# Kernel tuning notes

Hardware: AMD Instinct MI355X
Metric: run time of the kernel (lower is better)

## Reference

```python
import jax, jax.numpy as jnp
import numpy as np
from math import comb

B = 2048          # num_batch
NVAR = 11         # Bernstein coefficients per axis
NUM = 100         # trajectory time samples
NUM_OBS = 10
MAXITER = 50
T_FIN = 5.0
A_OBS = 0.4; B_OBS = 0.4
RHO_OBS = 1.0; RHO_INEQ = 1.0; RHO_TARGET = 1.0; RHO_PROJ = 1.0
V_MIN = 0.1; V_MAX = 2.0; A_MAX = 2.0


def _bernstein(n, t):
    return np.stack([comb(n, k) * t**k * (1.0 - t)**(n - k) for k in range(n + 1)], axis=1)


def _basis_matrices():
    # Bernstein polynomial basis of degree NVAR-1 sampled at NUM points over [0, T_FIN]
    t = np.linspace(0.0, 1.0, NUM)
    n = NVAR - 1
    P = _bernstein(n, t)
    Bm1 = _bernstein(n - 1, t)
    Bm2 = _bernstein(n - 2, t)
    dP = np.zeros_like(P); ddP = np.zeros_like(P)
    for k in range(n + 1):
        d = np.zeros(NUM)
        if k > 0: d += Bm1[:, k - 1]
        if k < n: d -= Bm1[:, k]
        dP[:, k] = n * d / T_FIN
        dd = np.zeros(NUM)
        if k > 1: dd += Bm2[:, k - 2]
        if 0 < k < n: dd -= 2.0 * Bm2[:, k - 1]
        if k < n - 1: dd += Bm2[:, k]
        ddP[:, k] = n * (n - 1) * dd / T_FIN**2
    return (jnp.asarray(P, jnp.float32), jnp.asarray(dP, jnp.float32), jnp.asarray(ddP, jnp.float32))


def setup_inputs() -> dict:
    key = jax.random.key(0)
    ks = jax.random.split(key, 10)
    P, Pdot, Pddot = _basis_matrices()
    u = lambda k, s, lo, hi: jax.random.uniform(k, s, jnp.float32, lo, hi)
    init_state_ego = jnp.concatenate([u(ks[0], (B, 2), -1.0, 1.0), u(ks[1], (B, 2), 0.1, 1.0)], axis=1)
    term_states = jnp.concatenate([u(ks[2], (B, 2), 2.0, 6.0), u(ks[3], (B, 2), 0.1, 1.0)], axis=1)
    via_points = u(ks[4], (B, 4), 0.5, 4.0)
    closest_obs = u(ks[5], (B, 2 * NUM_OBS), -4.0, 4.0)
    target_init = jnp.concatenate([u(ks[6], (B, 2), 1.0, 5.0), u(ks[7], (B, 2), -0.5, 0.5)], axis=1)
    d_min_t = u(ks[8], (B, 1), 1.0, 1.5)
    d_max_t = d_min_t + u(ks[9], (B, 1), 0.5, 1.0)
    d_target_bounds = jnp.concatenate([d_min_t, d_max_t], axis=1)
    return {"P": P, "Pdot": Pdot, "Pddot": Pddot, "init_state_ego": init_state_ego,
            "term_states": term_states, "via_points": via_points, "closest_obs": closest_obs,
            "target_init": target_init, "d_target_bounds": d_target_bounds}


def reference(P, Pdot, Pddot, init_state_ego, term_states, via_points, closest_obs, target_init, d_target_bounds):
    dt = P.dtype
    tot_time = jnp.linspace(0.0, T_FIN, NUM, dtype=dt)
    A_via = jnp.stack([P[49], P[74]])
    A_eq_init = jnp.vstack([P[0], Pdot[0], P[-1], Pdot[-1], A_via])   # [6, NVAR]
    A_eq = jnp.vstack([P[0], Pdot[0], P[-1], Pdot[-1]])               # [4, NVAR]
    A_obs_mat = jnp.tile(P, (NUM_OBS, 1))                             # [NUM_OBS*NUM, NVAR]
    A_vel, A_acc, A_target = Pdot, Pddot, P

    def kkt_inv(cost, A):
        m = A.shape[0]
        M = jnp.vstack([jnp.hstack([cost, A.T]), jnp.hstack([A, jnp.zeros((m, m), dt)])])
        return jnp.linalg.inv(M)

    inv_init = kkt_inv(Pddot.T @ Pddot, A_eq_init)
    cost_opt = (RHO_OBS * A_obs_mat.T @ A_obs_mat + RHO_INEQ * A_acc.T @ A_acc
                + RHO_INEQ * A_vel.T @ A_vel + RHO_TARGET * A_target.T @ A_target
                + RHO_PROJ * jnp.eye(NVAR, dtype=dt))
    inv_opt = kkt_inv(cost_opt, A_eq)

    zeros1 = jnp.zeros((B, 1), dt)
    vx0, vy0 = init_state_ego[:, 2:3], init_state_ego[:, 3:4]
    x_term, y_term = term_states[:, 0:1], term_states[:, 1:2]
    vx_term, vy_term = term_states[:, 2:3], term_states[:, 3:4]

    # warm-start QP (equality-constrained, zero linear cost): qp_layer_init
    b_eq_x_init = jnp.hstack([zeros1, vx0, x_term, vx_term, via_points[:, 0:2]])
    b_eq_y_init = jnp.hstack([zeros1, vy0, y_term, vy_term, via_points[:, 2:4]])
    zlin = jnp.zeros((B, NVAR), dt)
    c_x_bar = (jnp.hstack([zlin, b_eq_x_init]) @ inv_init.T)[:, :NVAR]
    c_y_bar = (jnp.hstack([zlin, b_eq_y_init]) @ inv_init.T)[:, :NVAR]

    b_eq_x = jnp.hstack([zeros1, vx0, x_term, vx_term])
    b_eq_y = jnp.hstack([zeros1, vy0, y_term, vy_term])

    # constant-velocity target trajectory, [B, NUM]
    x_target = target_init[:, 0:1] + target_init[:, 2:3] * tot_time[None, :]
    y_target = target_init[:, 1:2] + target_init[:, 3:4] * tot_time[None, :]

    # static obstacles tiled over time (obs-major, time fastest), [B, NUM_OBS*NUM]
    x_obs_traj = jnp.repeat(closest_obs[:, :NUM_OBS], NUM, axis=1)
    y_obs_traj = jnp.repeat(closest_obs[:, NUM_OBS:2 * NUM_OBS], NUM, axis=1)
    d_min_t, d_max_t = d_target_bounds[:, 0:1], d_target_bounds[:, 1:2]

    def step(carry, _):
        primal, lx, ly = carry
        cx, cy = primal[:, :NVAR], primal[:, NVAR:]
        x, xdot, xddot = cx @ P.T, cx @ Pdot.T, cx @ Pddot.T
        y, ydot, yddot = cy @ P.T, cy @ Pdot.T, cy @ Pddot.T
        # obstacle avoidance polar reformulation (compute_alph_d)
        wc = jnp.tile(x, (1, NUM_OBS)) - x_obs_traj
        ws = jnp.tile(y, (1, NUM_OBS)) - y_obs_traj
        a_o = jnp.arctan2(ws * A_OBS, wc * B_OBS)
        ca, sa = jnp.cos(a_o), jnp.sin(a_o)
        c1 = RHO_OBS * (A_OBS**2 * ca**2 + B_OBS**2 * sa**2)
        c2 = RHO_OBS * (A_OBS * wc * ca + B_OBS * ws * sa)
        d_obs = jnp.maximum(jnp.ones_like(c2), c2 / c1)
        # velocity bound (rho_ineq cancels in c2/c1)
        a_v = jnp.arctan2(ydot, xdot); cv, sv = jnp.cos(a_v), jnp.sin(a_v)
        d_v = jnp.clip(xdot * cv + ydot * sv, V_MIN, V_MAX)
        # acceleration bound
        a_a = jnp.arctan2(yddot, xddot); cA, sA = jnp.cos(a_a), jnp.sin(a_a)
        d_a = jnp.clip(xddot * cA + yddot * sA, 0.0, A_MAX)
        # target distance band
        wct, wst = x - x_target, y - y_target
        bt = jnp.arctan2(wst, wct); cb, sb = jnp.cos(bt), jnp.sin(bt)
        d_t = jnp.clip(wct * cb + wst * sb, d_min_t, d_max_t)
        # residuals -> dual (lambda) update
        res_xo = wc - A_OBS * d_obs * ca; res_yo = ws - B_OBS * d_obs * sa
        res_vx = xdot - d_v * cv;         res_vy = ydot - d_v * sv
        res_ax = xddot - d_a * cA;        res_ay = yddot - d_a * sA
        res_tx = wct - d_t * cb;          res_ty = wst - d_t * sb
        lx = lx - RHO_OBS * res_xo @ A_obs_mat - RHO_INEQ * res_ax @ A_acc - RHO_INEQ * res_vx @ A_vel - RHO_TARGET * res_tx @ A_target
        ly = ly - RHO_OBS * res_yo @ A_obs_mat - RHO_INEQ * res_ay @ A_acc - RHO_INEQ * res_vy @ A_vel - RHO_TARGET * res_ty @ A_target
        # linear cost and closed-form KKT solve (A_projection = I)
        b_ox = x_obs_traj + A_OBS * d_obs * ca; b_oy = y_obs_traj + B_OBS * d_obs * sa
        b_tx = x_target + d_t * cb;             b_ty = y_target + d_t * sb
        lin_x = (-lx - RHO_OBS * b_ox @ A_obs_mat - RHO_INEQ * (d_a * cA) @ A_acc
                 - RHO_INEQ * (d_v * cv) @ A_vel - RHO_TARGET * b_tx @ A_target - RHO_PROJ * c_x_bar)
        lin_y = (-ly - RHO_OBS * b_oy @ A_obs_mat - RHO_INEQ * (d_a * sA) @ A_acc
                 - RHO_INEQ * (d_v * sv) @ A_vel - RHO_TARGET * b_ty @ A_target - RHO_PROJ * c_y_bar)
        new_cx = (jnp.hstack([-lin_x, b_eq_x]) @ inv_opt.T)[:, :NVAR]
        new_cy = (jnp.hstack([-lin_y, b_eq_y]) @ inv_opt.T)[:, :NVAR]
        return (jnp.hstack([new_cx, new_cy]), lx, ly), None

    init = (jnp.hstack([c_x_bar, c_y_bar]), jnp.zeros((B, NVAR), dt), jnp.zeros((B, NVAR), dt))
    (primal, lx, ly), _ = jax.lax.scan(jax.checkpoint(step), init, None, length=MAXITER)
    return primal
```

## Files before the change

kernel.cpp:

```cpp
#include <hip/hip_runtime.h>
#include <math.h>

#define NVARS 11
#define NUMT  100
#define NOBS  10
#define MAXIT 50

#define E_OFF    0
#define F_OFF    66
#define G4_OFF   187
#define GP_OFF   231
#define GPD_OFF  352
#define GPDD_OFF 473
#define WS_FLOATS 594

#define BSTRIDE 308

__device__ void gj_inv(double (*aug)[34], int N, double* fac, int* piv, int tid, int nthr)
{
    for (int k = 0; k < N; ++k) {
        if (tid == 0) {
            int p = k; double best = fabs(aug[k][k]);
            for (int r = k + 1; r < N; ++r) { double v = fabs(aug[r][k]); if (v > best) { best = v; p = r; } }
            *piv = p;
        }
        __syncthreads();
        int p = *piv;
        if (p != k) {
            for (int c = tid; c < 2 * N; c += nthr) { double t = aug[k][c]; aug[k][c] = aug[p][c]; aug[p][c] = t; }
        }
        __syncthreads();
        double pv = aug[k][k];
        __syncthreads();
        for (int c = tid; c < 2 * N; c += nthr) aug[k][c] /= pv;
        __syncthreads();
        if (tid < N) fac[tid] = aug[tid][k];
        __syncthreads();
        for (int idx = tid; idx < N * 2 * N; idx += nthr) {
            int r = idx / (2 * N), c = idx % (2 * N);
            if (r != k) aug[r][c] -= fac[r] * aug[k][c];
        }
        __syncthreads();
    }
}

__global__ __launch_bounds__(128) void setup_kernel(const float* __restrict__ P,
                                                    const float* __restrict__ Pd,
                                                    const float* __restrict__ Pdd,
                                                    float* __restrict__ ws)
{
    __shared__ double G[3][NVARS][NVARS];
    __shared__ double aug[17][34];
    __shared__ double fac[17];
    __shared__ int piv;
    const int tid = threadIdx.x, nthr = 128;

    for (int idx = tid; idx < 3 * 121; idx += nthr) {
        int q = idx / 121, rem = idx % 121, r = rem / 11, c = rem % 11;
        const float* B = (q == 0) ? P : (q == 1) ? Pd : Pdd;
        double s = 0.0;
        for (int t = 0; t < NUMT; ++t) s += (double)B[t * 11 + r] * (double)B[t * 11 + c];
        G[q][r][c] = s;
    }
    __syncthreads();
    for (int idx = tid; idx < 3 * 121; idx += nthr) ws[GP_OFF + idx] = (float)((&G[0][0][0])[idx]);

    for (int idx = tid; idx < 17 * 34; idx += nthr) aug[idx / 34][idx % 34] = 0.0;
    __syncthreads();
    for (int idx = tid; idx < 121; idx += nthr) aug[idx / 11][idx % 11] = G[2][idx / 11][idx % 11];
    if (tid < 66) {
        int r = tid / 11, j = tid % 11;
        const float* src = (r == 0) ? P : (r == 1) ? Pd : (r == 2) ? (P + 99 * 11) : (r == 3) ? (Pd + 99 * 11)
                           : (r == 4) ? (P + 49 * 11) : (P + 74 * 11);
        double v = (double)src[j];
        aug[j][11 + r] = v;
        aug[11 + r][j] = v;
    }
    if (tid < 17) aug[tid][17 + tid] = 1.0;
    __syncthreads();
    gj_inv(aug, 17, fac, &piv, tid, nthr);
    if (tid < 66) { int j = tid / 6, k = tid % 6; ws[E_OFF + tid] = (float)aug[j][17 + 11 + k]; }
    __syncthreads();

    for (int idx = tid; idx < 17 * 34; idx += nthr) aug[idx / 34][idx % 34] = 0.0;
    __syncthreads();
    for (int idx = tid; idx < 121; idx += nthr) {
        int r = idx / 11, c = idx % 11;
        aug[r][c] = 11.0 * G[0][r][c] + G[1][r][c] + G[2][r][c] + ((r == c) ? 1.0 : 0.0);
    }
    if (tid < 44) {
        int r = tid / 11, j = tid % 11;
        const float* src = (r == 0) ? P : (r == 1) ? Pd : (r == 2) ? (P + 99 * 11) : (Pd + 99 * 11);
        double v = (double)src[j];
        aug[j][11 + r] = v;
        aug[11 + r][j] = v;
    }
    if (tid < 15) aug[tid][15 + tid] = 1.0;
    __syncthreads();
    gj_inv(aug, 15, fac, &piv, tid, nthr);
    if (tid < 121) { int j = tid / 11, k = tid % 11; ws[F_OFF + tid] = (float)aug[j][15 + k]; }
    if (tid < 44)  { int j = tid / 4,  k = tid % 4;  ws[G4_OFF + tid] = (float)aug[j][15 + 11 + k]; }
}

__device__ __forceinline__ float sbcast(float v) {
    return __int_as_float(__builtin_amdgcn_readfirstlane(__float_as_int(v)));
}

__global__ __launch_bounds__(128, 4) void solve_kernel(
    const float* __restrict__ P, const float* __restrict__ Pd, const float* __restrict__ Pdd,
    const float* __restrict__ ise, const float* __restrict__ term, const float* __restrict__ via,
    const float* __restrict__ obs, const float* __restrict__ tgt, const float* __restrict__ dtb,
    const float* __restrict__ ws, float* __restrict__ out)
{
    __shared__ __align__(16) float sBc[NVARS][BSTRIDE];
    __shared__ __align__(16) float wbc[2][BSTRIDE];
    __shared__ float cst[WS_FLOATS];
    __shared__ float sd456[3][24];
    __shared__ float Dred[6][12];
    __shared__ float mlin[2][12];
    __shared__ float scoef[2][12];
    __shared__ float beqs[2][4];
    __shared__ float sobs[2][NOBS];
    __shared__ float stgt[6];

    const int tid = threadIdx.x;
    const int b = blockIdx.x;

    for (int idx = tid; idx < NVARS * BSTRIDE; idx += 128) {
        int j = idx / BSTRIDE, r = idx % BSTRIDE;
        float v = 0.f;
        if (r < 300) {
            int q = r / 100, t = r % 100;
            const float* Bq = (q == 0) ? P : (q == 1) ? Pd : Pdd;
            v = Bq[t * 11 + j];
        }
        sBc[j][r] = v;
    }
    for (int idx = tid; idx < WS_FLOATS; idx += 128) cst[idx] = ws[idx];
    if (tid < 20) sobs[tid / 10][tid % 10] = obs[b * 20 + tid];
    if (tid == 0) {
        beqs[0][0] = 0.f; beqs[0][1] = ise[b*4+2]; beqs[0][2] = term[b*4+0]; beqs[0][3] = term[b*4+2];
        beqs[1][0] = 0.f; beqs[1][1] = ise[b*4+3]; beqs[1][2] = term[b*4+1]; beqs[1][3] = term[b*4+3];
        stgt[0] = tgt[b*4+0]; stgt[1] = tgt[b*4+2];
        stgt[2] = tgt[b*4+1]; stgt[3] = tgt[b*4+3];
        stgt[4] = dtb[b*2+0]; stgt[5] = dtb[b*2+1];
    }
    __syncthreads();

    const int ca = tid / 11, cj = tid % 11;
    float lm = 0.f, cb = 0.f;
    if (tid < 22) {
        float bi0 = 0.f, bi1 = beqs[ca][1], bi2 = beqs[ca][2], bi3 = beqs[ca][3];
        float bi4 = via[b*4 + 2*ca + 0], bi5 = via[b*4 + 2*ca + 1];
        const float* E = &cst[E_OFF + cj * 6];
        float s = E[0]*bi0 + E[1]*bi1 + E[2]*bi2 + E[3]*bi3 + E[4]*bi4 + E[5]*bi5;
        cb = s; scoef[ca][cj] = s;
    }

    float rP[NVARS], rPd[NVARS], rPdd[NVARS];
    {
        const int t = (tid < NUMT) ? tid : 0;
        #pragma unroll
        for (int k = 0; k < NVARS; ++k) {
            rP[k]   = sBc[k][t];
            rPd[k]  = sBc[k][t + 100];
            rPdd[k] = sBc[k][t + 200];
        }
    }
    float obx[NOBS], oby[NOBS];
    #pragma unroll
    for (int o = 0; o < NOBS; ++o) {
        obx[o] = sbcast(sobs[0][o]);
        oby[o] = sbcast(sobs[1][o]);
    }
    const float tg0 = sbcast(stgt[0]), tg1 = sbcast(stgt[1]);
    const float tg2 = sbcast(stgt[2]), tg3 = sbcast(stgt[3]);
    const float tg4 = sbcast(stgt[4]), tg5 = sbcast(stgt[5]);

    float* pwA = &wbc[0][tid];
    const int lg = tid - 100;

    int btask = -1;
    if (tid <= 32) btask = tid;
    else if (tid >= 64 && tid <= 96) btask = tid - 31;
    const int wi = (btask >= 0) ? btask % 6 : 0;
    const int bjj = (btask >= 0) ? btask / 6 : 0;
    const float4* pbB = (const float4*)(&sBc[0][0] + bjj * BSTRIDE + (wi % 3) * 100);
    const float4* pwB = (const float4*)(&wbc[wi / 3][(wi % 3) * 100]);
    __syncthreads();

    for (int it = 0; it < MAXIT; ++it) {
        if (tid < NUMT) {
            float x=0,y=0,xd=0,yd=0,xdd=0,ydd=0;
            #pragma unroll
            for (int k = 0; k < NVARS; ++k) {
                float cxk = scoef[0][k], cyk = scoef[1][k];
                x += cxk*rP[k];   y += cyk*rP[k];
                xd += cxk*rPd[k]; yd += cyk*rPd[k];
                xdd += cxk*rPdd[k]; ydd += cyk*rPdd[k];
            }
            float Sbx = 0.f, Sby = 0.f;
            #pragma unroll
            for (int o = 0; o < NOBS; ++o) {
                float dx = x - obx[o], dy = y - oby[o];
                float r2 = dx*dx + dy*dy;
                float f  = fmaxf(1.0f, 0.4f * rsqrtf(fmaxf(r2, 1e-30f)));
                Sbx += fmaf(dx, f, obx[o]);
                Sby += fmaf(dy, f, oby[o]);
            }
            float rv = sqrtf(xd*xd + yd*yd);
            float fv = fminf(fmaxf(rv, 0.1f), 2.0f) / fmaxf(rv, 1e-30f);
            float ra = sqrtf(xdd*xdd + ydd*ydd);
            float fa = fminf(ra, 2.0f) / fmaxf(ra, 1e-30f);
            float tt = (float)tid * (5.0f / 99.0f);
            float xt = tg0 + tg1*tt, yt = tg2 + tg3*tt;
            float wct = x - xt, wst = y - yt;
            float rt = sqrtf(wct*wct + wst*wst);
            float ftg = fminf(fmaxf(rt, tg4), tg5) / fmaxf(rt, 1e-30f);
            pwA[0]   = Sbx + xt + wct*ftg;
            pwA[100] = xd * fv;
            pwA[200] = xdd * fa;
            pwA[BSTRIDE]       = Sby + yt + wst*ftg;
            pwA[BSTRIDE + 100] = yd * fv;
            pwA[BSTRIDE + 200] = ydd * fa;
        }
        if (lg >= 0 && lg < 22) {
            const int ga = lg / 11, gj = lg % 11;
            float d4=0.f, d5=0.f, d6=0.f;
            #pragma unroll
            for (int k = 0; k < 11; ++k) {
                float ck = scoef[ga][k];
                d4 += ck * cst[GP_OFF   + k*11 + gj];
                d5 += ck * cst[GPD_OFF  + k*11 + gj];
                d6 += ck * cst[GPDD_OFF + k*11 + gj];
            }
            sd456[0][lg] = d4; sd456[1][lg] = d5; sd456[2][lg] = d6;
        }
        __syncthreads();

        if (btask >= 0) {
            float s = 0.f;
            #pragma unroll
            for (int i = 0; i < 25; ++i) {
                float4 a = pbB[i], w = pwB[i];
                s += w.x * a.x; s += w.y * a.y; s += w.z * a.z; s += w.w * a.w;
            }
            Dred[wi][bjj] = s;
        }
        __syncthreads();

        if (tid < 22) {
            float d4 = sd456[0][tid], d5 = sd456[1][tid], d6 = sd456[2][tid];
            int i0 = 3*ca;
            float D0 = Dred[i0][cj], D1 = Dred[i0+1][cj], D2 = Dred[i0+2][cj];
            lm -= (11.f*d4 - D0) + (d5 - D1) + (d6 - D2);
            mlin[ca][cj] = lm + D0 + D1 + D2 + cb;
        }

        if (tid < 22) {
            float s = 0.f;
            #pragma unroll
            for (int k = 0; k < 11; ++k) s += cst[F_OFF + cj*11 + k] * mlin[ca][k];
            #pragma unroll
            for (int k = 0; k < 4; ++k)  s += cst[G4_OFF + cj*4 + k] * beqs[ca][k];
            scoef[ca][cj] = s;
        }
        __syncthreads();
    }

    if (tid < 22) out[b * 22 + tid] = scoef[ca][cj];
}

extern "C" void kernel_launch(void* const* d_in, const int* in_sizes, int n_in,
                              void* d_out, int out_size, void* d_ws, size_t ws_size,
                              hipStream_t stream)
{
    const float* P    = (const float*)d_in[0];
    const float* Pd   = (const float*)d_in[1];
    const float* Pdd  = (const float*)d_in[2];
    const float* ise  = (const float*)d_in[3];
    const float* term = (const float*)d_in[4];
    const float* via  = (const float*)d_in[5];
    const float* obs  = (const float*)d_in[6];
    const float* tgt  = (const float*)d_in[7];
    const float* dtb  = (const float*)d_in[8];
    float* ws  = (float*)d_ws;
    float* out = (float*)d_out;

    const int B = in_sizes[3] / 4;

    hipLaunchKernelGGL(setup_kernel, dim3(1), dim3(128), 0, stream, P, Pd, Pdd, ws);
    hipLaunchKernelGGL(solve_kernel, dim3(B), dim3(128), 0, stream,
                       P, Pd, Pdd, ise, term, via, obs, tgt, dtb, ws, out);
}
```

Before: 240.7 us.

## Split Bernstein reduction dot products across all threads in two halves

The 66 length-100 reduction dot products were computed by 66 threads, each doing 25 float4 iterations. Now every one of the 128 threads computes half of a dot product (12-13 float4s), with four threads taking an extra half, and the partial sums go to shared memory and are added in the coefficient update. The d4/d5/d6 and coefficient-update work also moves from threads 0-21 to threads 100-121, so those values stay in registers and one shared buffer goes away. This shortens the critical path of the reduction stage at the cost of a few extra shared-memory reads and some index arithmetic.

Measured after the change: 246.8 us. 1.03x slower.

```diff
diff --git a/kernel.cpp b/kernel.cpp
--- a/kernel.cpp
+++ b/kernel.cpp
@@ -115,8 +115,7 @@
     __shared__ __align__(16) float sBc[NVARS][BSTRIDE];
     __shared__ __align__(16) float wbc[2][BSTRIDE];
     __shared__ float cst[WS_FLOATS];
-    __shared__ float sd456[3][24];
-    __shared__ float Dred[6][12];
+    __shared__ float pS[136];
     __shared__ float mlin[2][12];
     __shared__ float scoef[2][12];
     __shared__ float beqs[2][4];
@@ -147,9 +146,11 @@
     }
     __syncthreads();
 
-    const int ca = tid / 11, cj = tid % 11;
+    const int lc = tid - 100;
+    const int ca = (lc >= 0) ? lc / 11 : 0, cj = (lc >= 0) ? lc % 11 : 0;
+
     float lm = 0.f, cb = 0.f;
-    if (tid < 22) {
+    if (lc >= 0 && lc < 22) {
         float bi0 = 0.f, bi1 = beqs[ca][1], bi2 = beqs[ca][2], bi3 = beqs[ca][3];
         float bi4 = via[b*4 + 2*ca + 0], bi5 = via[b*4 + 2*ca + 1];
         const float* E = &cst[E_OFF + cj * 6];
@@ -178,16 +179,22 @@
     const float tg4 = sbcast(stgt[4]), tg5 = sbcast(stgt[5]);
 
     float* pwA = &wbc[0][tid];
-    const int lg = tid - 100;
-
-    int btask = -1;
-    if (tid <= 32) btask = tid;
-    else if (tid >= 64 && tid <= 96) btask = tid - 31;
-    const int wi = (btask >= 0) ? btask % 6 : 0;
-    const int bjj = (btask >= 0) ? btask / 6 : 0;
-    const float4* pbB = (const float4*)(&sBc[0][0] + bjj * BSTRIDE + (wi % 3) * 100);
-    const float4* pwB = (const float4*)(&wbc[wi / 3][(wi % 3) * 100]);
-    __syncthreads();
+
+    const int sB   = tid;
+    const int taskB = (sB < 66) ? sB : sB - 66;
+    const int halfB = (sB < 66) ? 0 : 1;
+    const int wiB = taskB % 6, bjB = taskB / 6;
+    const float4* pbB = (const float4*)(&sBc[0][0] + bjB * BSTRIDE + (wiB % 3) * 100) + (halfB ? 13 : 0);
+    const float4* pwB = (const float4*)(&wbc[wiB / 3][(wiB % 3) * 100]) + (halfB ? 13 : 0);
+    const int ccB = halfB ? 12 : 13;
+    const bool has2 = (tid >= 60 && tid < 64);
+    const int task2 = 62 + (tid - 60);
+    const int wi2 = task2 % 6, bj2 = task2 / 6;
+    const float4* pb2 = (const float4*)(&sBc[0][0] + bj2 * BSTRIDE + (wi2 % 3) * 100) + 13;
+    const float4* pw2 = (const float4*)(&wbc[wi2 / 3][(wi2 % 3) * 100]) + 13;
+    __syncthreads();
+
+    float d4 = 0.f, d5 = 0.f, d6 = 0.f;
 
     for (int it = 0; it < MAXIT; ++it) {
         if (tid < NUMT) {
@@ -224,40 +231,54 @@
             pwA[BSTRIDE + 100] = yd * fv;
             pwA[BSTRIDE + 200] = ydd * fa;
         }
-        if (lg >= 0 && lg < 22) {
-            const int ga = lg / 11, gj = lg % 11;
-            float d4=0.f, d5=0.f, d6=0.f;
+        if (lc >= 0 && lc < 22) {
+            float a4=0.f, a5=0.f, a6=0.f;
             #pragma unroll
             for (int k = 0; k < 11; ++k) {
-                float ck = scoef[ga][k];
-                d4 += ck * cst[GP_OFF   + k*11 + gj];
-                d5 += ck * cst[GPD_OFF  + k*11 + gj];
-                d6 += ck * cst[GPDD_OFF + k*11 + gj];
-            }
-            sd456[0][lg] = d4; sd456[1][lg] = d5; sd456[2][lg] = d6;
-        }
-        __syncthreads();
-
-        if (btask >= 0) {
+                float ck = scoef[ca][k];
+                a4 += ck * cst[GP_OFF   + k*11 + cj];
+                a5 += ck * cst[GPD_OFF  + k*11 + cj];
+                a6 += ck * cst[GPDD_OFF + k*11 + cj];
+            }
+            d4 = a4; d5 = a5; d6 = a6;
+        }
+        __syncthreads();
+
+        {
             float s = 0.f;
             #pragma unroll
-            for (int i = 0; i < 25; ++i) {
-                float4 a = pbB[i], w = pwB[i];
+            for (int i = 0; i < 13; ++i) {
+                if (i < ccB) {
+                    float4 a = pbB[i], w = pwB[i];
+                    s += w.x * a.x; s += w.y * a.y; s += w.z * a.z; s += w.w * a.w;
+                }
+            }
+            pS[sB] = s;
+        }
+        if (has2) {
+            float s = 0.f;
+            #pragma unroll
+            for (int i = 0; i < 12; ++i) {
+                float4 a = pb2[i], w = pw2[i];
                 s += w.x * a.x; s += w.y * a.y; s += w.z * a.z; s += w.w * a.w;
             }
-            Dred[wi][bjj] = s;
-        }
-        __syncthreads();
-
-        if (tid < 22) {
-            float d4 = sd456[0][tid], d5 = sd456[1][tid], d6 = sd456[2][tid];
-            int i0 = 3*ca;
-            float D0 = Dred[i0][cj], D1 = Dred[i0+1][cj], D2 = Dred[i0+2][cj];
+            pS[128 + (tid - 60)] = s;
+        }
+        __syncthreads();
+
+        if (lc >= 0 && lc < 22) {
+            int t0 = cj * 6 + 3 * ca;
+            int h1_0 = (t0 + 0 < 62) ? (66 + t0 + 0) : (128 + (t0 + 0 - 62));
+            int h1_1 = (t0 + 1 < 62) ? (66 + t0 + 1) : (128 + (t0 + 1 - 62));
+            int h1_2 = (t0 + 2 < 62) ? (66 + t0 + 2) : (128 + (t0 + 2 - 62));
+            float D0 = pS[t0 + 0] + pS[h1_0];
+            float D1 = pS[t0 + 1] + pS[h1_1];
+            float D2 = pS[t0 + 2] + pS[h1_2];
             lm -= (11.f*d4 - D0) + (d5 - D1) + (d6 - D2);
             mlin[ca][cj] = lm + D0 + D1 + D2 + cb;
         }
 
-        if (tid < 22) {
+        if (lc >= 0 && lc < 22) {
             float s = 0.f;
             #pragma unroll
             for (int k = 0; k < 11; ++k) s += cst[F_OFF + cj*11 + k] * mlin[ca][k];
@@ -268,7 +289,7 @@
         __syncthreads();
     }
 
-    if (tid < 22) out[b * 22 + tid] = scoef[ca][cj];
+    if (lc >= 0 && lc < 22) out[b * 22 + lc] = scoef[ca][cj];
 }
 
 extern "C" void kernel_launch(void* const* d_in, const int* in_sizes, int n_in,
```
